# Kernel tuning notes

Measured on AMD Instinct MI355X. Metric: run time of the kernel, lower is better.

## Reference

```python
import jax, jax.numpy as jnp
import numpy as np

N_TERMS = 26000
N_EDGES = 120000
BATCH = 64
N_FEAT = 14          # n_base_models + 4
GO_EMB = 8
HID = 64
IN_DIM = N_FEAT + GO_EMB  # 22


def setup_inputs() -> dict:
    key = jax.random.key(0)
    ks = jax.random.split(key, 12)
    s = 0.05
    return {
        "x": jax.random.normal(ks[0], (BATCH, N_TERMS, N_FEAT), jnp.float32),
        "edge_index": jax.random.randint(ks[1], (2, N_EDGES), 0, N_TERMS, jnp.int32),
        "term_indices": jnp.arange(N_TERMS, dtype=jnp.int32),
        "emb_table": jax.random.normal(ks[2], (N_TERMS, GO_EMB), jnp.float32),
        "W1": jax.random.normal(ks[3], (HID, IN_DIM), jnp.float32) * s,
        "b1": jnp.zeros((HID,), jnp.float32),
        "W2": jax.random.normal(ks[4], (HID, HID), jnp.float32) * s,
        "b2": jnp.zeros((HID,), jnp.float32),
        "W3": jax.random.normal(ks[5], (HID // 2, HID), jnp.float32) * s,
        "b3": jnp.zeros((HID // 2,), jnp.float32),
        "Wout": jax.random.normal(ks[6], (1, HID // 2), jnp.float32) * s,
        "bout": jnp.zeros((1,), jnp.float32),
    }


def _go_conv(x, row, col, deg_inv, W, b):
    # x: [B, N, C]. Mean-aggregate neighbor features (col -> row), add self, linear.
    agg = jnp.zeros_like(x).at[:, row].add(x[:, col])        # scatter_add over edges
    agg = agg * deg_inv[None, :, None]
    return jnp.einsum('bnc,oc->bno', x + agg, W) + b


def reference(x, edge_index, term_indices, emb_table, W1, b1, W2, b2, W3, b3, Wout, bout):
    B, N, _ = x.shape
    row, col = edge_index[0], edge_index[1]
    deg = jnp.zeros((N,), x.dtype).at[row].add(1.0)
    deg_inv = 1.0 / jnp.clip(deg, 1.0)

    go_emb = emb_table[term_indices]                          # [N, GO_EMB]
    h = jnp.concatenate([x, jnp.broadcast_to(go_emb[None], (B, N, go_emb.shape[-1]))], axis=-1)

    h = jax.nn.relu(_go_conv(h, row, col, deg_inv, W1, b1))   # dropout: eval mode (identity)
    h = jax.nn.relu(_go_conv(h, row, col, deg_inv, W2, b2))
    h = jax.nn.relu(_go_conv(h, row, col, deg_inv, W3, b3))
    out = jax.nn.sigmoid(jnp.einsum('bnc,oc->bno', h, Wout) + bout)  # [B, N, 1]
    return out[..., 0]
```

## Files before the change

kernel.cpp:

```cpp
#include <hip/hip_runtime.h>
#include <stdint.h>

static constexpr int NT = 26000;
static constexpr int NE = 120000;

typedef __attribute__((ext_vector_type(8))) short short8;
typedef __attribute__((ext_vector_type(4))) float f32x4;
typedef __attribute__((ext_vector_type(4))) unsigned int u32x4;

__device__ __forceinline__ int rfl(int v){ return __builtin_amdgcn_readfirstlane(v); }

__device__ __forceinline__ float bf_lo(uint32_t u){ union{uint32_t u; float f;} a; a.u = u<<16; return a.f; }
__device__ __forceinline__ float bf_hi(uint32_t u){ union{uint32_t u; float f;} a; a.u = u & 0xffff0000u; return a.f; }
__device__ __forceinline__ uint32_t f2b(float f){ union{float f; uint32_t u;} a; a.f=f; return (a.u + 0x7fffu + ((a.u>>16)&1u))>>16; }

__device__ __forceinline__ void nts4(uint8_t* p, uint32_t a, uint32_t b, uint32_t c, uint32_t d){
  u32x4 v; v.x=a; v.y=b; v.z=c; v.w=d;
  __builtin_nontemporal_store(v, reinterpret_cast<u32x4*>(p));
}

__global__ __launch_bounds__(256) void k_zero_deg(int* __restrict__ deg){
  int i = blockIdx.x*256 + threadIdx.x;
  if (i < NT) deg[i] = 0;
}
__global__ __launch_bounds__(256) void k_count(const int* __restrict__ ei, int* __restrict__ deg){
  int e = blockIdx.x*256 + threadIdx.x;
  if (e < NE) atomicAdd(&deg[ei[e]], 1);
}
__global__ __launch_bounds__(1024) void k_scan(const int* __restrict__ deg, int* __restrict__ rp,
                                               int* __restrict__ cur){
  __shared__ int part[1024];
  const int t = threadIdx.x;
  const int CH = (NT + 1023)/1024;
  const int base = t*CH;
  int sum = 0;
  for (int i=0;i<CH;i++){
    int idx=base+i;
    if (idx<NT){ int d = deg[idx]; sum += (d<=4)?4:((d+3)&~3); }
  }
  part[t] = sum;
  __syncthreads();
  for (int off=1; off<1024; off<<=1){
    int v = (t>=off) ? part[t-off] : 0;
    __syncthreads();
    part[t] += v;
    __syncthreads();
  }
  int run = (t==0) ? 0 : part[t-1];
  for (int i=0;i<CH;i++){
    int idx = base+i;
    if (idx<NT){
      int d = deg[idx];
      int slot = (d<=4)?4:((d+3)&~3);
      rp[idx] = run; cur[idx] = run;
      run += slot;
    }
  }
  if (t==1023) rp[NT] = part[1023];
}
__global__ __launch_bounds__(256) void k_init(uint32_t* __restrict__ zp, uint32_t* __restrict__ cols32,
                                              float* __restrict__ scP, float* __restrict__ scQ,
                                              float* __restrict__ scY){
  int i = blockIdx.x*256 + threadIdx.x;
  if (i < 1024) zp[i] = 0;
  else if (i < 1024 + 112004) cols32[i-1024] = 0x65906590u;
  if (i < 2){ scP[NT*2+i] = 0.f; scQ[NT*2+i] = 0.f; scY[NT*2+i] = 0.f; }
}
__global__ __launch_bounds__(256) void k_fill(const int* __restrict__ ei, int* __restrict__ cur,
                                              uint16_t* __restrict__ cols){
  int e = blockIdx.x*256 + threadIdx.x;
  if (e < NE){
    int r = ei[e];
    int pos = atomicAdd(&cur[r], 1);
    cols[pos] = (uint16_t)ei[NE + e];
  }
}
__global__ __launch_bounds__(256) void k_prepw(const float* __restrict__ W1, const float* __restrict__ W2,
                                               const float* __restrict__ W3,
                                               uint16_t* __restrict__ Wt1, uint16_t* __restrict__ Wt2,
                                               uint16_t* __restrict__ Wt3){
  for (int idx = threadIdx.x; idx < 8192; idx += 256){
    if (idx < 2048){
      int o = idx >> 5, k = idx & 31;
      Wt1[idx] = (uint16_t)((k < 22) ? f2b(W1[o*22 + k]) : 0);
    } else if (idx < 6144){
      int j = idx - 2048;
      Wt2[j] = (uint16_t)f2b(W2[j]);
    } else {
      int j = idx - 6144;
      Wt3[j] = (uint16_t)f2b(W3[j]);
    }
  }
}

__global__ __launch_bounds__(256) void k_build_h0(const float* __restrict__ x, const int* __restrict__ tidx,
                                                  const float* __restrict__ emb,
                                                  uint8_t* __restrict__ p8, float* __restrict__ scP){
  __shared__ float red[2][16][16];
  __shared__ float sinv[2][16];
  const int t  = threadIdx.x;
  const int ni = t & 15;
  const int n  = blockIdx.x*16 + ni;
  const int r  = t >> 4;
  const float* er = emb + (size_t)tidx[n]*8;
  float ev[8];
  #pragma unroll
  for (int i=0;i<8;i++) ev[i]=er[i];

  float v[2][32];
  #pragma unroll
  for (int rt=0; rt<2; rt++){
    const int b = r + rt*16;
    const float* xr = x + ((size_t)b*NT + n)*14;
    float m = 0.f;
    #pragma unroll
    for (int i=0;i<14;i++){ float a=xr[i]; v[rt][i]=a; m=fmaxf(m,fabsf(a)); }
    #pragma unroll
    for (int i=0;i<8;i++){ float a=ev[i]; v[rt][14+i]=a; m=fmaxf(m,fabsf(a)); }
    #pragma unroll
    for (int i=22;i<32;i++) v[rt][i]=0.f;
    red[rt][r][ni] = m;
  }
  __syncthreads();
  if (t < 32){
    int rt = t >> 4, nn = t & 15;
    float mm = 0.f;
    #pragma unroll
    for (int i=0;i<16;i++) mm = fmaxf(mm, red[rt][i][nn]);
    sinv[rt][nn] = (mm > 0.f) ? 127.0f/mm : 0.f;
    scP[(size_t)(blockIdx.x*16+nn)*2 + rt] = mm * (1.0f/127.0f);
  }
  __syncthreads();

  uint8_t* dst = p8 + (size_t)n*1024;
  #pragma unroll
  for (int rt=0; rt<2; rt++){
    const float inv = sinv[rt][ni];
    uint32_t pk[8];
    #pragma unroll
    for (int u=0;u<8;u++){
      uint32_t w = 0;
      #pragma unroll
      for (int j=0;j<4;j++){
        int q = __float2int_rn(v[rt][u*4+j]*inv) + 128;
        q = q < 0 ? 0 : (q > 255 ? 255 : q);
        w |= (uint32_t)q << (8*j);
      }
      pk[u] = w;
    }
    nts4(dst + rt*512 + r*32,      pk[0],pk[1],pk[2],pk[3]);
    nts4(dst + rt*512 + r*32 + 16, pk[4],pk[5],pk[6],pk[7]);
  }
}

template<int KS> struct VecT;
template<> struct VecT<2>{ using T = uint4; };
template<> struct VecT<1>{ using T = uint2; };

__device__ __forceinline__ void dq_u(float* a, uint32_t u, float s){
  a[0] += s*(float)(u & 0xffu);
  a[1] += s*(float)((u>>8) & 0xffu);
  a[2] += s*(float)((u>>16) & 0xffu);
  a[3] += s*(float)(u>>24);
}
__device__ __forceinline__ void dq_s(float* a, uint32_t u, float s){
  a[0] += s*(float)(int8_t)(u & 0xff);
  a[1] += s*(float)(int8_t)((u>>8) & 0xff);
  a[2] += s*(float)(int8_t)((u>>16) & 0xff);
  a[3] += s*(float)(int8_t)(u>>24);
}
template<int KS, bool SG>
__device__ __forceinline__ void dqv(float (&acc)[KS][8], const typename VecT<KS>::T& v, float s){
  if constexpr (KS==2){
    if constexpr (SG){ dq_s(&acc[0][0],v.x,s); dq_s(&acc[0][4],v.y,s); dq_s(&acc[1][0],v.z,s); dq_s(&acc[1][4],v.w,s); }
    else             { dq_u(&acc[0][0],v.x,s); dq_u(&acc[0][4],v.y,s); dq_u(&acc[1][0],v.z,s); dq_u(&acc[1][4],v.w,s); }
  } else {
    if constexpr (SG){ dq_s(&acc[0][0],v.x,s); dq_s(&acc[0][4],v.y,s); }
    else             { dq_u(&acc[0][0],v.x,s); dq_u(&acc[0][4],v.y,s); }
  }
}

template<int KS, int STRB, int MODE>
__device__ __forceinline__ float aggregate_q(float (&acc)[KS][8], float& sumS,
    const uint8_t* __restrict__ hin, const uint8_t* __restrict__ zp8,
    const float* __restrict__ sc,
    const int* __restrict__ rp, const int* __restrict__ cur,
    const uint16_t* __restrict__ cols, int node, uint32_t offB, int rt)
{
  using V = typename VecT<KS>::T;
  constexpr bool SG = (MODE==2);
  const int e0 = rfl(rp[node]);
  const int e1 = rfl(rp[node+1]);
  const int dg = rfl(cur[node]) - e0;

  uint2 cc0 = *reinterpret_cast<const uint2*>(cols + e0);
  int a0 = rfl(cc0.x), a1 = rfl(cc0.y);
  int c0 = a0 & 0xffff, c1 = (a0>>16) & 0xffff, c2 = a1 & 0xffff, c3 = (a1>>16) & 0xffff;
  auto bp = [&](int c)->const uint8_t*{ return (c < NT) ? (hin + (size_t)c*STRB) : zp8; };

  V v0 = *reinterpret_cast<const V*>(bp(c0) + offB); float s0 = sc[c0*2+rt];
  V v1 = *reinterpret_cast<const V*>(bp(c1) + offB); float s1 = sc[c1*2+rt];
  V v2 = *reinterpret_cast<const V*>(bp(c2) + offB); float s2 = sc[c2*2+rt];
  V v3 = *reinterpret_cast<const V*>(bp(c3) + offB); float s3 = sc[c3*2+rt];
  V ow = *reinterpret_cast<const V*>(hin + (size_t)node*STRB + offB);
  float so = sc[node*2+rt];
  uint2 ccA = *reinterpret_cast<const uint2*>(cols + e0 + 4);

  const float degf = (float)(dg > 1 ? dg : 1);
  #pragma unroll
  for (int ks=0;ks<KS;ks++)
    #pragma unroll
    for (int j=0;j<8;j++) acc[ks][j]=0.f;
  dqv<KS,SG>(acc, ow, so*degf);
  if constexpr (MODE==1) sumS = so*degf;

  for (int e = e0; e < e1; e += 4){
    uint2 ccN = *reinterpret_cast<const uint2*>(cols + e + 8);
    int p0 = rfl(ccA.x), p1 = rfl(ccA.y);
    int n0 = (e+4 < e1) ? (p0 & 0xffff)         : NT;
    int n1 = (e+5 < e1) ? ((p0 >> 16) & 0xffff) : NT;
    int n2 = (e+6 < e1) ? (p1 & 0xffff)         : NT;
    int n3 = (e+7 < e1) ? ((p1 >> 16) & 0xffff) : NT;
    dqv<KS,SG>(acc, v0, s0); if constexpr (MODE==1) sumS += s0;
    v0 = *reinterpret_cast<const V*>(bp(n0) + offB); s0 = sc[n0*2+rt];
    dqv<KS,SG>(acc, v1, s1); if constexpr (MODE==1) sumS += s1;
    v1 = *reinterpret_cast<const V*>(bp(n1) + offB); s1 = sc[n1*2+rt];
    dqv<KS,SG>(acc, v2, s2); if constexpr (MODE==1) sumS += s2;
    v2 = *reinterpret_cast<const V*>(bp(n2) + offB); s2 = sc[n2*2+rt];
    dqv<KS,SG>(acc, v3, s3); if constexpr (MODE==1) sumS += s3;
    v3 = *reinterpret_cast<const V*>(bp(n3) + offB); s3 = sc[n3*2+rt];
    ccA = ccN;
  }
  return 1.0f / degf;
}

__global__ __launch_bounds__(256, 8) void k_layer1(
    const uint8_t* __restrict__ pin, const float* __restrict__ scP,
    uint8_t* __restrict__ qout, float* __restrict__ scQ,
    const int* __restrict__ rp, const int* __restrict__ cur,
    const uint16_t* __restrict__ cols, const uint8_t* __restrict__ zp8,
    const uint16_t* __restrict__ Wt, const float* __restrict__ bias)
{
  const int t=threadIdx.x, lane=t&63, w=t>>6, l15=lane&15, lg=lane>>4;
  const int rt = w & 1;
  const int node = blockIdx.x*2 + (w>>1);

  const uint32_t offB = (uint32_t)(rt*512 + l15*32 + lg*8);

  float acc[1][8]; float sumS = 0.f;
  const float di = aggregate_q<1,1024,1>(acc, sumS, pin, zp8, scP, rp, cur, cols, node, offB, rt);
  const float corr = 128.0f * sumS;

  short8 bfrag;
  #pragma unroll
  for (int j=0;j<8;j++) bfrag[j] = (short)f2b((acc[0][j] - corr)*di);

  float av[4][4];
  float m = 0.f;
  #pragma unroll
  for (int ot=0;ot<4;ot++){
    const int o0 = ot*16;
    short8 af = *reinterpret_cast<const short8*>(Wt + (o0 + l15)*32 + lg*8);
    f32x4 d = *reinterpret_cast<const f32x4*>(bias + o0 + lg*4);
    d = __builtin_amdgcn_mfma_f32_16x16x32_bf16(af, bfrag, d, 0,0,0);
    #pragma unroll
    for (int j=0;j<4;j++){
      float v = fmaxf(d[j], 0.f);
      av[ot][j] = v;
      m = fmaxf(m, v);
    }
  }
  #pragma unroll
  for (int sh=1; sh<64; sh<<=1) m = fmaxf(m, __shfl_xor(m, sh, 64));
  const float inv = (m > 0.f) ? 255.0f/m : 0.f;

  uint8_t* base = qout + (size_t)node*2048 + rt*1024 + l15*64;
  #pragma unroll
  for (int ot=0;ot<4;ot++){
    uint32_t pk = 0;
    #pragma unroll
    for (int j=0;j<4;j++){
      int q = __float2int_rn(av[ot][j]*inv);
      q = q > 255 ? 255 : q;
      pk |= (uint32_t)q << (8*j);
    }
    uint32_t boff = ((((ot&1)<<1)|(lg>>1))<<4) + ((ot>>1)<<3) + ((lg&1)<<2);
    __builtin_nontemporal_store(pk, reinterpret_cast<uint32_t*>(base + boff));
  }
  if (lane == 0) scQ[node*2+rt] = m * (1.0f/255.0f);
}

__global__ __launch_bounds__(256, 6) void k_l2g3(
    const uint8_t* __restrict__ qin, const float* __restrict__ scQ,
    uint8_t* __restrict__ yout, float* __restrict__ scY,
    const int* __restrict__ rp, const int* __restrict__ cur,
    const uint16_t* __restrict__ cols, const uint8_t* __restrict__ zp8,
    const uint16_t* __restrict__ Wt2, const float* __restrict__ bias,
    const uint16_t* __restrict__ Wt3)
{
  __shared__ uint32_t lt[4*512];
  const int t=threadIdx.x, lane=t&63, w=t>>6, l15=lane&15, lg=lane>>4;
  const int rt = w & 1;
  const int node = blockIdx.x*2 + (w>>1);

  const uint32_t offB = (uint32_t)(rt*1024 + l15*64 + lg*16);

  float acc[2][8]; float dummy;
  const float di = aggregate_q<2,2048,0>(acc, dummy, qin, zp8, scQ, rp, cur, cols, node, offB, rt);

  short8 bfrag[2];
  #pragma unroll
  for (int ks=0;ks<2;ks++){
    short8 bf;
    #pragma unroll
    for (int j=0;j<8;j++) bf[j] = (short)f2b(acc[ks][j]*di);
    bfrag[ks]=bf;
  }

  uint32_t* L = lt + w*512;
  #pragma unroll
  for (int ot=0;ot<4;ot++){
    const int o0 = ot*16;
    short8 af0 = *reinterpret_cast<const short8*>(Wt2 + (o0 + l15)*64 + lg*8);
    short8 af1 = *reinterpret_cast<const short8*>(Wt2 + (o0 + l15)*64 + 32 + lg*8);
    f32x4 d = *reinterpret_cast<const f32x4*>(bias + o0 + lg*4);
    d = __builtin_amdgcn_mfma_f32_16x16x32_bf16(af0, bfrag[0], d, 0,0,0);
    d = __builtin_amdgcn_mfma_f32_16x16x32_bf16(af1, bfrag[1], d, 0,0,0);
    float a0=fmaxf(d[0],0.f), a1=fmaxf(d[1],0.f), a2=fmaxf(d[2],0.f), a3=fmaxf(d[3],0.f);
    *reinterpret_cast<uint2*>(L + ot*128 + l15*8 + lg*2) =
        make_uint2(f2b(a0) | (f2b(a1)<<16), f2b(a2) | (f2b(a3)<<16));
  }

  short8 b3f[2];
  #pragma unroll
  for (int ks=0;ks<2;ks++)
    b3f[ks] = *reinterpret_cast<const short8*>(L + (ks*2+(lg>>1))*128 + l15*8 + (lg&1)*4);

  float dd[2][4];
  float m = 0.f;
  #pragma unroll
  for (int ot=0;ot<2;ot++){
    const int o0 = ot*16;
    short8 af0 = *reinterpret_cast<const short8*>(Wt3 + (o0 + l15)*64 + lg*8);
    short8 af1 = *reinterpret_cast<const short8*>(Wt3 + (o0 + l15)*64 + 32 + lg*8);
    f32x4 d = {0.f,0.f,0.f,0.f};
    d = __builtin_amdgcn_mfma_f32_16x16x32_bf16(af0, b3f[0], d, 0,0,0);
    d = __builtin_amdgcn_mfma_f32_16x16x32_bf16(af1, b3f[1], d, 0,0,0);
    #pragma unroll
    for (int j=0;j<4;j++){
      dd[ot][j] = d[j];
      m = fmaxf(m, fabsf(d[j]));
    }
  }
  #pragma unroll
  for (int sh=1; sh<64; sh<<=1) m = fmaxf(m, __shfl_xor(m, sh, 64));
  const float inv = (m > 0.f) ? 127.0f/m : 0.f;

  uint8_t* base = yout + (size_t)node*1024 + rt*512 + l15*32;
  #pragma unroll
  for (int ot=0;ot<2;ot++){
    uint32_t pk = 0;
    #pragma unroll
    for (int j=0;j<4;j++){
      int q = __float2int_rn(dd[ot][j]*inv);
      pk |= (uint32_t)(q & 0xff) << (8*j);
    }
    uint32_t boff = (((ot<<1)|(lg>>1))<<3) + ((lg&1)<<2);
    __builtin_nontemporal_store(pk, reinterpret_cast<uint32_t*>(base + boff));
  }
  if (lane == 0) scY[node*2+rt] = m * (1.0f/127.0f);
}

__global__ __launch_bounds__(256, 8) void k_fin(
    const uint8_t* __restrict__ yin, const float* __restrict__ scY,
    const int* __restrict__ rp, const int* __restrict__ cur,
    const uint16_t* __restrict__ cols, const uint8_t* __restrict__ zp8,
    const float* __restrict__ b3, const float* __restrict__ Wo, const float* __restrict__ bo,
    float* __restrict__ tmp)
{
  const int t=threadIdx.x, lane=t&63, w=t>>6, l15=lane&15, lg=lane>>4;
  const int rt = w & 1;
  const int node = blockIdx.x*2 + (w>>1);

  const uint32_t offB = (uint32_t)(rt*512 + l15*32 + lg*8);

  float acc[1][8]; float dummy;
  const float di = aggregate_q<1,1024,2>(acc, dummy, yin, zp8, scY, rp, cur, cols, node, offB, rt);

  const int k0 = lg*8;
  f32x4 bA = *reinterpret_cast<const f32x4*>(b3 + k0);
  f32x4 bB = *reinterpret_cast<const f32x4*>(b3 + k0 + 4);
  f32x4 wA = *reinterpret_cast<const f32x4*>(Wo + k0);
  f32x4 wB = *reinterpret_cast<const f32x4*>(Wo + k0 + 4);
  float z = 0.f;
  #pragma unroll
  for (int j=0;j<4;j++){
    z += fmaxf(acc[0][j]  *di + bA[j], 0.f) * wA[j];
    z += fmaxf(acc[0][4+j]*di + bB[j], 0.f) * wB[j];
  }
  z += __shfl_xor(z, 16, 64);
  z += __shfl_xor(z, 32, 64);
  if (lg == 0){
    float sg = 1.f/(1.f + expf(-(z + bo[0])));
    tmp[(size_t)node*32 + rt*16 + l15] = sg;
  }
}

__global__ __launch_bounds__(256) void k_tr(const float* __restrict__ tmp, float* __restrict__ out){
  int n = blockIdx.x*256 + threadIdx.x;
  if (n < NT){
    f32x4 r[8];
    #pragma unroll
    for (int q=0;q<8;q++) r[q] = *reinterpret_cast<const f32x4*>(tmp + (size_t)n*32 + q*4);
    #pragma unroll
    for (int q=0;q<8;q++)
      #pragma unroll
      for (int j=0;j<4;j++)
        out[(size_t)(q*4+j)*NT + n] = r[q][j];
  }
}

static constexpr size_t OFF_P    = 0;
static constexpr size_t OFF_Q    = 26624000;
static constexpr size_t OFF_TMP  = 79872000;
static constexpr size_t OFF_ZP   = 83200000;
static constexpr size_t OFF_WT1  = OFF_ZP  + 4096;
static constexpr size_t OFF_WT2  = OFF_WT1 + 4096;
static constexpr size_t OFF_WT3  = OFF_WT2 + 8192;
static constexpr size_t OFF_SCP  = OFF_WT3 + 4096;
static constexpr size_t OFF_SCQ  = OFF_SCP + 208016;
static constexpr size_t OFF_SCY  = OFF_SCQ + 208016;
static constexpr size_t OFF_DEG  = OFF_SCY + 208016;
static constexpr size_t OFF_RP   = OFF_DEG + 104000;
static constexpr size_t OFF_CUR  = OFF_RP  + 104016;
static constexpr size_t OFF_COLS = OFF_CUR + 104000;
static constexpr size_t WS_NEED  = OFF_COLS + 448016;

extern "C" void kernel_launch(void* const* d_in, const int* in_sizes, int n_in,
                              void* d_out, int out_size, void* d_ws, size_t ws_size,
                              hipStream_t stream)
{
  const float* x    = (const float*)d_in[0];
  const int*   ei   = (const int*)  d_in[1];
  const int*   tidx = (const int*)  d_in[2];
  const float* emb  = (const float*)d_in[3];
  const float* W1   = (const float*)d_in[4];
  const float* b1   = (const float*)d_in[5];
  const float* W2   = (const float*)d_in[6];
  const float* b2   = (const float*)d_in[7];
  const float* W3   = (const float*)d_in[8];
  const float* b3   = (const float*)d_in[9];
  const float* Wo   = (const float*)d_in[10];
  const float* bo   = (const float*)d_in[11];
  float* out = (float*)d_out;

  if (ws_size < WS_NEED) return;

  char* ws = (char*)d_ws;
  uint8_t*  P    = (uint8_t*) (ws + OFF_P);
  uint8_t*  Y3   = (uint8_t*) (ws + OFF_P);
  uint8_t*  Q    = (uint8_t*) (ws + OFF_Q);
  float*    tmpf = (float*)   (ws + OFF_TMP);
  uint32_t* zp   = (uint32_t*)(ws + OFF_ZP);
  uint8_t*  zp8  = (uint8_t*) (ws + OFF_ZP);
  uint16_t* Wt1  = (uint16_t*)(ws + OFF_WT1);
  uint16_t* Wt2  = (uint16_t*)(ws + OFF_WT2);
  uint16_t* Wt3  = (uint16_t*)(ws + OFF_WT3);
  float*    scP  = (float*)   (ws + OFF_SCP);
  float*    scQ  = (float*)   (ws + OFF_SCQ);
  float*    scY  = (float*)   (ws + OFF_SCY);
  int*      deg  = (int*)     (ws + OFF_DEG);
  int*      rp   = (int*)     (ws + OFF_RP);
  int*      cur  = (int*)     (ws + OFF_CUR);
  uint16_t* cols = (uint16_t*)(ws + OFF_COLS);

  k_zero_deg<<<(NT+255)/256, 256, 0, stream>>>(deg);
  k_count   <<<(NE+255)/256, 256, 0, stream>>>(ei, deg);
  k_scan    <<<1, 1024, 0, stream>>>(deg, rp, cur);
  k_init    <<<442, 256, 0, stream>>>(zp, (uint32_t*)cols, scP, scQ, scY);
  k_fill    <<<(NE+255)/256, 256, 0, stream>>>(ei, cur, cols);
  k_prepw   <<<1, 256, 0, stream>>>(W1, W2, W3, Wt1, Wt2, Wt3);

  for (int ch = 0; ch < 2; ch++){
    k_build_h0<<<NT/16, 256, 0, stream>>>(x + (size_t)ch*32*NT*14, tidx, emb, P, scP);
    k_layer1<<<NT/2, 256, 0, stream>>>(P, scP, Q, scQ, rp, cur, cols, zp8, Wt1, b1);
    k_l2g3  <<<NT/2, 256, 0, stream>>>(Q, scQ, Y3, scY, rp, cur, cols, zp8, Wt2, b2, Wt3);
    k_fin   <<<NT/2, 256, 0, stream>>>(Y3, scY, rp, cur, cols, zp8, b3, Wo, bo, tmpf);
    k_tr    <<<(NT+255)/256, 256, 0, stream>>>(tmpf, out + (size_t)ch*32*NT);
  }
}
```

Before: 501.0 us.

## Merge batch chunks into single launches and store first 16 neighbors per node in fixed slots

New measurement: 507.8 us. Within noise of the previous version (+1.4%).

```diff
diff --git a/kernel.cpp b/kernel.cpp
--- a/kernel.cpp
+++ b/kernel.cpp
@@ -8,10 +8,10 @@
 typedef __attribute__((ext_vector_type(4))) float f32x4;
 typedef __attribute__((ext_vector_type(4))) unsigned int u32x4;
 
+static constexpr int SCS = 52004;
+
 __device__ __forceinline__ int rfl(int v){ return __builtin_amdgcn_readfirstlane(v); }
 
-__device__ __forceinline__ float bf_lo(uint32_t u){ union{uint32_t u; float f;} a; a.u = u<<16; return a.f; }
-__device__ __forceinline__ float bf_hi(uint32_t u){ union{uint32_t u; float f;} a; a.u = u & 0xffff0000u; return a.f; }
 __device__ __forceinline__ uint32_t f2b(float f){ union{float f; uint32_t u;} a; a.f=f; return (a.u + 0x7fffu + ((a.u>>16)&1u))>>16; }
 
 __device__ __forceinline__ void nts4(uint8_t* p, uint32_t a, uint32_t b, uint32_t c, uint32_t d){
@@ -59,20 +59,31 @@
   if (t==1023) rp[NT] = part[1023];
 }
 __global__ __launch_bounds__(256) void k_init(uint32_t* __restrict__ zp, uint32_t* __restrict__ cols32,
+                                              uint32_t* __restrict__ cols2_32,
                                               float* __restrict__ scP, float* __restrict__ scQ,
                                               float* __restrict__ scY){
   int i = blockIdx.x*256 + threadIdx.x;
   if (i < 1024) zp[i] = 0;
-  else if (i < 1024 + 112004) cols32[i-1024] = 0x65906590u;
-  if (i < 2){ scP[NT*2+i] = 0.f; scQ[NT*2+i] = 0.f; scY[NT*2+i] = 0.f; }
+  else if (i < 113028) cols32[i-1024] = 0x65906590u;
+  else if (i < 321028) cols2_32[i-113028] = 0x65906590u;
+  if (i < 4){
+    int ch = i>>1, j = i&1;
+    scP[ch*SCS + NT*2 + j] = 0.f;
+    scQ[ch*SCS + NT*2 + j] = 0.f;
+    scY[ch*SCS + NT*2 + j] = 0.f;
+  }
 }
 __global__ __launch_bounds__(256) void k_fill(const int* __restrict__ ei, int* __restrict__ cur,
-                                              uint16_t* __restrict__ cols){
+                                              const int* __restrict__ rp,
+                                              uint16_t* __restrict__ cols, uint16_t* __restrict__ cols2){
   int e = blockIdx.x*256 + threadIdx.x;
   if (e < NE){
     int r = ei[e];
     int pos = atomicAdd(&cur[r], 1);
-    cols[pos] = (uint16_t)ei[NE + e];
+    int slot = pos - rp[r];
+    uint16_t c = (uint16_t)ei[NE + e];
+    if (slot < 16) cols2[r*16 + slot] = c;
+    else           cols[pos] = c;
   }
 }
 __global__ __launch_bounds__(256) void k_prepw(const float* __restrict__ W1, const float* __restrict__ W2,
@@ -98,9 +109,16 @@
                                                   uint8_t* __restrict__ p8, float* __restrict__ scP){
   __shared__ float red[2][16][16];
   __shared__ float sinv[2][16];
+  const int nb16 = NT/16;
+  const int ch = (blockIdx.x >= nb16) ? 1 : 0;
+  const int bi = blockIdx.x - ch*nb16;
+  const float* xc = x + (size_t)ch*32*NT*14;
+  uint8_t* p8c = p8 + (size_t)ch*NT*1024;
+  float* scc = scP + (size_t)ch*SCS;
+
   const int t  = threadIdx.x;
   const int ni = t & 15;
-  const int n  = blockIdx.x*16 + ni;
+  const int n  = bi*16 + ni;
   const int r  = t >> 4;
   const float* er = emb + (size_t)tidx[n]*8;
   float ev[8];
@@ -111,7 +129,7 @@
   #pragma unroll
   for (int rt=0; rt<2; rt++){
     const int b = r + rt*16;
-    const float* xr = x + ((size_t)b*NT + n)*14;
+    const float* xr = xc + ((size_t)b*NT + n)*14;
     float m = 0.f;
     #pragma unroll
     for (int i=0;i<14;i++){ float a=xr[i]; v[rt][i]=a; m=fmaxf(m,fabsf(a)); }
@@ -128,11 +146,11 @@
     #pragma unroll
     for (int i=0;i<16;i++) mm = fmaxf(mm, red[rt][i][nn]);
     sinv[rt][nn] = (mm > 0.f) ? 127.0f/mm : 0.f;
-    scP[(size_t)(blockIdx.x*16+nn)*2 + rt] = mm * (1.0f/127.0f);
+    scc[(size_t)(bi*16+nn)*2 + rt] = mm * (1.0f/127.0f);
   }
   __syncthreads();
 
-  uint8_t* dst = p8 + (size_t)n*1024;
+  uint8_t* dst = p8c + (size_t)n*1024;
   #pragma unroll
   for (int rt=0; rt<2; rt++){
     const float inv = sinv[rt][ni];
@@ -181,32 +199,37 @@
 }
 
 template<int KS, int STRB, int MODE>
-__device__ __forceinline__ float aggregate_q(float (&acc)[KS][8], float& sumS,
+__device__ __forceinline__ float aggregate8(float (&acc)[KS][8], float& sumS,
     const uint8_t* __restrict__ hin, const uint8_t* __restrict__ zp8,
     const float* __restrict__ sc,
-    const int* __restrict__ rp, const int* __restrict__ cur,
-    const uint16_t* __restrict__ cols, int node, uint32_t offB, int rt)
+    const int* __restrict__ deg, const int* __restrict__ rp,
+    const uint16_t* __restrict__ cols, const uint16_t* __restrict__ cols2,
+    int node, uint32_t offB, int rt)
 {
   using V = typename VecT<KS>::T;
   constexpr bool SG = (MODE==2);
-  const int e0 = rfl(rp[node]);
-  const int e1 = rfl(rp[node+1]);
-  const int dg = rfl(cur[node]) - e0;
-
-  uint2 cc0 = *reinterpret_cast<const uint2*>(cols + e0);
-  int a0 = rfl(cc0.x), a1 = rfl(cc0.y);
-  int c0 = a0 & 0xffff, c1 = (a0>>16) & 0xffff, c2 = a1 & 0xffff, c3 = (a1>>16) & 0xffff;
   auto bp = [&](int c)->const uint8_t*{ return (c < NT) ? (hin + (size_t)c*STRB) : zp8; };
 
-  V v0 = *reinterpret_cast<const V*>(bp(c0) + offB); float s0 = sc[c0*2+rt];
-  V v1 = *reinterpret_cast<const V*>(bp(c1) + offB); float s1 = sc[c1*2+rt];
-  V v2 = *reinterpret_cast<const V*>(bp(c2) + offB); float s2 = sc[c2*2+rt];
-  V v3 = *reinterpret_cast<const V*>(bp(c3) + offB); float s3 = sc[c3*2+rt];
+  const uint4 cc0 = *reinterpret_cast<const uint4*>(cols2 + node*16);
+  const uint4 cc1 = *reinterpret_cast<const uint4*>(cols2 + node*16 + 8);
+  const int dg = rfl(deg[node]);
   V ow = *reinterpret_cast<const V*>(hin + (size_t)node*STRB + offB);
-  float so = sc[node*2+rt];
-  uint2 ccA = *reinterpret_cast<const uint2*>(cols + e0 + 4);
-
-  const float degf = (float)(dg > 1 ? dg : 1);
+  const float so = sc[node*2+rt];
+
+  int c0 = rfl(cc0.x)&0xffff, c1 = (rfl(cc0.x)>>16)&0xffff;
+  int c2 = rfl(cc0.y)&0xffff, c3 = (rfl(cc0.y)>>16)&0xffff;
+  int c4 = rfl(cc0.z)&0xffff, c5 = (rfl(cc0.z)>>16)&0xffff;
+  int c6 = rfl(cc0.w)&0xffff, c7 = (rfl(cc0.w)>>16)&0xffff;
+  V v0 = *reinterpret_cast<const V*>(bp(c0)+offB); float s0 = sc[c0*2+rt];
+  V v1 = *reinterpret_cast<const V*>(bp(c1)+offB); float s1 = sc[c1*2+rt];
+  V v2 = *reinterpret_cast<const V*>(bp(c2)+offB); float s2 = sc[c2*2+rt];
+  V v3 = *reinterpret_cast<const V*>(bp(c3)+offB); float s3 = sc[c3*2+rt];
+  V v4 = *reinterpret_cast<const V*>(bp(c4)+offB); float s4 = sc[c4*2+rt];
+  V v5 = *reinterpret_cast<const V*>(bp(c5)+offB); float s5 = sc[c5*2+rt];
+  V v6 = *reinterpret_cast<const V*>(bp(c6)+offB); float s6 = sc[c6*2+rt];
+  V v7 = *reinterpret_cast<const V*>(bp(c7)+offB); float s7 = sc[c7*2+rt];
+
+  const float degf = (dg > 1) ? (float)dg : 1.0f;
   #pragma unroll
   for (int ks=0;ks<KS;ks++)
     #pragma unroll
@@ -214,41 +237,77 @@
   dqv<KS,SG>(acc, ow, so*degf);
   if constexpr (MODE==1) sumS = so*degf;
 
-  for (int e = e0; e < e1; e += 4){
-    uint2 ccN = *reinterpret_cast<const uint2*>(cols + e + 8);
-    int p0 = rfl(ccA.x), p1 = rfl(ccA.y);
-    int n0 = (e+4 < e1) ? (p0 & 0xffff)         : NT;
-    int n1 = (e+5 < e1) ? ((p0 >> 16) & 0xffff) : NT;
-    int n2 = (e+6 < e1) ? (p1 & 0xffff)         : NT;
-    int n3 = (e+7 < e1) ? ((p1 >> 16) & 0xffff) : NT;
-    dqv<KS,SG>(acc, v0, s0); if constexpr (MODE==1) sumS += s0;
-    v0 = *reinterpret_cast<const V*>(bp(n0) + offB); s0 = sc[n0*2+rt];
-    dqv<KS,SG>(acc, v1, s1); if constexpr (MODE==1) sumS += s1;
-    v1 = *reinterpret_cast<const V*>(bp(n1) + offB); s1 = sc[n1*2+rt];
-    dqv<KS,SG>(acc, v2, s2); if constexpr (MODE==1) sumS += s2;
-    v2 = *reinterpret_cast<const V*>(bp(n2) + offB); s2 = sc[n2*2+rt];
-    dqv<KS,SG>(acc, v3, s3); if constexpr (MODE==1) sumS += s3;
-    v3 = *reinterpret_cast<const V*>(bp(n3) + offB); s3 = sc[n3*2+rt];
-    ccA = ccN;
+  dqv<KS,SG>(acc, v0, s0); dqv<KS,SG>(acc, v1, s1);
+  dqv<KS,SG>(acc, v2, s2); dqv<KS,SG>(acc, v3, s3);
+  if constexpr (MODE==1) sumS += s0+s1+s2+s3;
+  if (dg > 4){
+    dqv<KS,SG>(acc, v4, s4); dqv<KS,SG>(acc, v5, s5);
+    dqv<KS,SG>(acc, v6, s6); dqv<KS,SG>(acc, v7, s7);
+    if constexpr (MODE==1) sumS += s4+s5+s6+s7;
+  }
+  if (dg > 8){
+    int c8  = rfl(cc1.x)&0xffff, c9  = (rfl(cc1.x)>>16)&0xffff;
+    int c10 = rfl(cc1.y)&0xffff, c11 = (rfl(cc1.y)>>16)&0xffff;
+    V w0 = *reinterpret_cast<const V*>(bp(c8)+offB);  float t0 = sc[c8*2+rt];
+    V w1 = *reinterpret_cast<const V*>(bp(c9)+offB);  float t1 = sc[c9*2+rt];
+    V w2 = *reinterpret_cast<const V*>(bp(c10)+offB); float t2 = sc[c10*2+rt];
+    V w3 = *reinterpret_cast<const V*>(bp(c11)+offB); float t3 = sc[c11*2+rt];
+    dqv<KS,SG>(acc, w0, t0); dqv<KS,SG>(acc, w1, t1);
+    dqv<KS,SG>(acc, w2, t2); dqv<KS,SG>(acc, w3, t3);
+    if constexpr (MODE==1) sumS += t0+t1+t2+t3;
+    if (dg > 12){
+      int c12 = rfl(cc1.z)&0xffff, c13 = (rfl(cc1.z)>>16)&0xffff;
+      int c14 = rfl(cc1.w)&0xffff, c15 = (rfl(cc1.w)>>16)&0xffff;
+      V y0 = *reinterpret_cast<const V*>(bp(c12)+offB); float u0 = sc[c12*2+rt];
+      V y1 = *reinterpret_cast<const V*>(bp(c13)+offB); float u1 = sc[c13*2+rt];
+      V y2 = *reinterpret_cast<const V*>(bp(c14)+offB); float u2 = sc[c14*2+rt];
+      V y3 = *reinterpret_cast<const V*>(bp(c15)+offB); float u3 = sc[c15*2+rt];
+      dqv<KS,SG>(acc, y0, u0); dqv<KS,SG>(acc, y1, u1);
+      dqv<KS,SG>(acc, y2, u2); dqv<KS,SG>(acc, y3, u3);
+      if constexpr (MODE==1) sumS += u0+u1+u2+u3;
+      if (dg > 16){
+        const int e0 = rfl(rp[node]);
+        const int slots = (dg+3)&~3;
+        for (int e = 16; e < slots; e += 4){
+          uint2 cx = *reinterpret_cast<const uint2*>(cols + e0 + e);
+          int d0 = rfl(cx.x)&0xffff, d1 = (rfl(cx.x)>>16)&0xffff;
+          int d2 = rfl(cx.y)&0xffff, d3 = (rfl(cx.y)>>16)&0xffff;
+          V z0 = *reinterpret_cast<const V*>(bp(d0)+offB); float q0 = sc[d0*2+rt];
+          V z1 = *reinterpret_cast<const V*>(bp(d1)+offB); float q1 = sc[d1*2+rt];
+          V z2 = *reinterpret_cast<const V*>(bp(d2)+offB); float q2 = sc[d2*2+rt];
+          V z3 = *reinterpret_cast<const V*>(bp(d3)+offB); float q3 = sc[d3*2+rt];
+          dqv<KS,SG>(acc, z0, q0); dqv<KS,SG>(acc, z1, q1);
+          dqv<KS,SG>(acc, z2, q2); dqv<KS,SG>(acc, z3, q3);
+          if constexpr (MODE==1) sumS += q0+q1+q2+q3;
+        }
+      }
+    }
   }
   return 1.0f / degf;
 }
 
-__global__ __launch_bounds__(256, 8) void k_layer1(
+__global__ __launch_bounds__(256, 6) void k_layer1(
     const uint8_t* __restrict__ pin, const float* __restrict__ scP,
     uint8_t* __restrict__ qout, float* __restrict__ scQ,
-    const int* __restrict__ rp, const int* __restrict__ cur,
-    const uint16_t* __restrict__ cols, const uint8_t* __restrict__ zp8,
+    const int* __restrict__ deg, const int* __restrict__ rp,
+    const uint16_t* __restrict__ cols, const uint16_t* __restrict__ cols2,
+    const uint8_t* __restrict__ zp8,
     const uint16_t* __restrict__ Wt, const float* __restrict__ bias)
 {
   const int t=threadIdx.x, lane=t&63, w=t>>6, l15=lane&15, lg=lane>>4;
   const int rt = w & 1;
-  const int node = blockIdx.x*2 + (w>>1);
+  const int idx = blockIdx.x*2 + (w>>1);
+  const int ch = (idx >= NT) ? 1 : 0;
+  const int node = idx - ch*NT;
+  const uint8_t* pc = pin + (size_t)ch*NT*1024;
+  uint8_t* qc = qout + (size_t)ch*NT*2048;
+  const float* scp = scP + (size_t)ch*SCS;
+  float* scq = scQ + (size_t)ch*SCS;
 
   const uint32_t offB = (uint32_t)(rt*512 + l15*32 + lg*8);
 
   float acc[1][8]; float sumS = 0.f;
-  const float di = aggregate_q<1,1024,1>(acc, sumS, pin, zp8, scP, rp, cur, cols, node, offB, rt);
+  const float di = aggregate8<1,1024,1>(acc, sumS, pc, zp8, scp, deg, rp, cols, cols2, node, offB, rt);
   const float corr = 128.0f * sumS;
 
   short8 bfrag;
@@ -274,7 +333,7 @@
   for (int sh=1; sh<64; sh<<=1) m = fmaxf(m, __shfl_xor(m, sh, 64));
   const float inv = (m > 0.f) ? 255.0f/m : 0.f;
 
-  uint8_t* base = qout + (size_t)node*2048 + rt*1024 + l15*64;
+  uint8_t* base = qc + (size_t)node*2048 + rt*1024 + l15*64;
   #pragma unroll
   for (int ot=0;ot<4;ot++){
     uint32_t pk = 0;
@@ -287,26 +346,33 @@
     uint32_t boff = ((((ot&1)<<1)|(lg>>1))<<4) + ((ot>>1)<<3) + ((lg&1)<<2);
     __builtin_nontemporal_store(pk, reinterpret_cast<uint32_t*>(base + boff));
   }
-  if (lane == 0) scQ[node*2+rt] = m * (1.0f/255.0f);
-}
-
-__global__ __launch_bounds__(256, 6) void k_l2g3(
+  if (lane == 0) scq[node*2+rt] = m * (1.0f/255.0f);
+}
+
+__global__ __launch_bounds__(256, 4) void k_l2g3(
     const uint8_t* __restrict__ qin, const float* __restrict__ scQ,
     uint8_t* __restrict__ yout, float* __restrict__ scY,
-    const int* __restrict__ rp, const int* __restrict__ cur,
-    const uint16_t* __restrict__ cols, const uint8_t* __restrict__ zp8,
+    const int* __restrict__ deg, const int* __restrict__ rp,
+    const uint16_t* __restrict__ cols, const uint16_t* __restrict__ cols2,
+    const uint8_t* __restrict__ zp8,
     const uint16_t* __restrict__ Wt2, const float* __restrict__ bias,
     const uint16_t* __restrict__ Wt3)
 {
   __shared__ uint32_t lt[4*512];
   const int t=threadIdx.x, lane=t&63, w=t>>6, l15=lane&15, lg=lane>>4;
   const int rt = w & 1;
-  const int node = blockIdx.x*2 + (w>>1);
+  const int idx = blockIdx.x*2 + (w>>1);
+  const int ch = (idx >= NT) ? 1 : 0;
+  const int node = idx - ch*NT;
+  const uint8_t* qc = qin + (size_t)ch*NT*2048;
+  uint8_t* yc = yout + (size_t)ch*NT*1024;
+  const float* scq = scQ + (size_t)ch*SCS;
+  float* scy = scY + (size_t)ch*SCS;
 
   const uint32_t offB = (uint32_t)(rt*1024 + l15*64 + lg*16);
 
   float acc[2][8]; float dummy;
-  const float di = aggregate_q<2,2048,0>(acc, dummy, qin, zp8, scQ, rp, cur, cols, node, offB, rt);
+  const float di = aggregate8<2,2048,0>(acc, dummy, qc, zp8, scq, deg, rp, cols, cols2, node, offB, rt);
 
   short8 bfrag[2];
   #pragma unroll
@@ -356,7 +422,7 @@
   for (int sh=1; sh<64; sh<<=1) m = fmaxf(m, __shfl_xor(m, sh, 64));
   const float inv = (m > 0.f) ? 127.0f/m : 0.f;
 
-  uint8_t* base = yout + (size_t)node*1024 + rt*512 + l15*32;
+  uint8_t* base = yc + (size_t)node*1024 + rt*512 + l15*32;
   #pragma unroll
   for (int ot=0;ot<2;ot++){
     uint32_t pk = 0;
@@ -368,24 +434,29 @@
     uint32_t boff = (((ot<<1)|(lg>>1))<<3) + ((lg&1)<<2);
     __builtin_nontemporal_store(pk, reinterpret_cast<uint32_t*>(base + boff));
   }
-  if (lane == 0) scY[node*2+rt] = m * (1.0f/127.0f);
-}
-
-__global__ __launch_bounds__(256, 8) void k_fin(
+  if (lane == 0) scy[node*2+rt] = m * (1.0f/127.0f);
+}
+
+__global__ __launch_bounds__(256, 6) void k_fin(
     const uint8_t* __restrict__ yin, const float* __restrict__ scY,
-    const int* __restrict__ rp, const int* __restrict__ cur,
-    const uint16_t* __restrict__ cols, const uint8_t* __restrict__ zp8,
+    const int* __restrict__ deg, const int* __restrict__ rp,
+    const uint16_t* __restrict__ cols, const uint16_t* __restrict__ cols2,
+    const uint8_t* __restrict__ zp8,
     const float* __restrict__ b3, const float* __restrict__ Wo, const float* __restrict__ bo,
     float* __restrict__ tmp)
 {
   const int t=threadIdx.x, lane=t&63, w=t>>6, l15=lane&15, lg=lane>>4;
   const int rt = w & 1;
-  const int node = blockIdx.x*2 + (w>>1);
+  const int idx = blockIdx.x*2 + (w>>1);
+  const int ch = (idx >= NT) ? 1 : 0;
+  const int node = idx - ch*NT;
+  const uint8_t* yc = yin + (size_t)ch*NT*1024;
+  const float* scy = scY + (size_t)ch*SCS;
 
   const uint32_t offB = (uint32_t)(rt*512 + l15*32 + lg*8);
 
   float acc[1][8]; float dummy;
-  const float di = aggregate_q<1,1024,2>(acc, dummy, yin, zp8, scY, rp, cur, cols, node, offB, rt);
+  const float di = aggregate8<1,1024,2>(acc, dummy, yc, zp8, scy, deg, rp, cols, cols2, node, offB, rt);
 
   const int k0 = lg*8;
   f32x4 bA = *reinterpret_cast<const f32x4*>(b3 + k0);
@@ -402,39 +473,45 @@
   z += __shfl_xor(z, 32, 64);
   if (lg == 0){
     float sg = 1.f/(1.f + expf(-(z + bo[0])));
-    tmp[(size_t)node*32 + rt*16 + l15] = sg;
+    tmp[(size_t)ch*NT*32 + (size_t)node*32 + rt*16 + l15] = sg;
   }
 }
 
 __global__ __launch_bounds__(256) void k_tr(const float* __restrict__ tmp, float* __restrict__ out){
-  int n = blockIdx.x*256 + threadIdx.x;
+  const int nb = (NT + 255)/256;
+  const int ch = (blockIdx.x >= nb) ? 1 : 0;
+  const int bi = blockIdx.x - ch*nb;
+  int n = bi*256 + threadIdx.x;
   if (n < NT){
+    const float* tc = tmp + (size_t)ch*NT*32;
+    float* oc = out + (size_t)ch*32*NT;
     f32x4 r[8];
     #pragma unroll
-    for (int q=0;q<8;q++) r[q] = *reinterpret_cast<const f32x4*>(tmp + (size_t)n*32 + q*4);
+    for (int q=0;q<8;q++) r[q] = *reinterpret_cast<const f32x4*>(tc + (size_t)n*32 + q*4);
     #pragma unroll
     for (int q=0;q<8;q++)
       #pragma unroll
       for (int j=0;j<4;j++)
-        out[(size_t)(q*4+j)*NT + n] = r[q][j];
-  }
-}
-
-static constexpr size_t OFF_P    = 0;
-static constexpr size_t OFF_Q    = 26624000;
-static constexpr size_t OFF_TMP  = 79872000;
-static constexpr size_t OFF_ZP   = 83200000;
-static constexpr size_t OFF_WT1  = OFF_ZP  + 4096;
-static constexpr size_t OFF_WT2  = OFF_WT1 + 4096;
-static constexpr size_t OFF_WT3  = OFF_WT2 + 8192;
-static constexpr size_t OFF_SCP  = OFF_WT3 + 4096;
-static constexpr size_t OFF_SCQ  = OFF_SCP + 208016;
-static constexpr size_t OFF_SCY  = OFF_SCQ + 208016;
-static constexpr size_t OFF_DEG  = OFF_SCY + 208016;
-static constexpr size_t OFF_RP   = OFF_DEG + 104000;
-static constexpr size_t OFF_CUR  = OFF_RP  + 104016;
-static constexpr size_t OFF_COLS = OFF_CUR + 104000;
-static constexpr size_t WS_NEED  = OFF_COLS + 448016;
+        oc[(size_t)(q*4+j)*NT + n] = r[q][j];
+  }
+}
+
+static constexpr size_t OFF_P     = 0;
+static constexpr size_t OFF_Q     = 53248000;
+static constexpr size_t OFF_TMP   = 159744000;
+static constexpr size_t OFF_ZP    = 166400000;
+static constexpr size_t OFF_WT1   = 166404096;
+static constexpr size_t OFF_WT2   = 166408192;
+static constexpr size_t OFF_WT3   = 166416384;
+static constexpr size_t OFF_SCP   = 166420480;
+static constexpr size_t OFF_SCQ   = 166836512;
+static constexpr size_t OFF_SCY   = 167252544;
+static constexpr size_t OFF_DEG   = 167668576;
+static constexpr size_t OFF_RP    = 167772576;
+static constexpr size_t OFF_CUR   = 167876592;
+static constexpr size_t OFF_COLS  = 167980592;
+static constexpr size_t OFF_COLS2 = 168428608;
+static constexpr size_t WS_NEED   = 169260608;
 
 extern "C" void kernel_launch(void* const* d_in, const int* in_sizes, int n_in,
                               void* d_out, int out_size, void* d_ws, size_t ws_size,
@@ -457,35 +534,34 @@
   if (ws_size < WS_NEED) return;
 
   char* ws = (char*)d_ws;
-  uint8_t*  P    = (uint8_t*) (ws + OFF_P);
-  uint8_t*  Y3   = (uint8_t*) (ws + OFF_P);
-  uint8_t*  Q    = (uint8_t*) (ws + OFF_Q);
-  float*    tmpf = (float*)   (ws + OFF_TMP);
-  uint32_t* zp   = (uint32_t*)(ws + OFF_ZP);
-  uint8_t*  zp8  = (uint8_t*) (ws + OFF_ZP);
-  uint16_t* Wt1  = (uint16_t*)(ws + OFF_WT1);
-  uint16_t* Wt2  = (uint16_t*)(ws + OFF_WT2);
-  uint16_t* Wt3  = (uint16_t*)(ws + OFF_WT3);
-  float*    scP  = (float*)   (ws + OFF_SCP);
-  float*    scQ  = (float*)   (ws + OFF_SCQ);
-  float*    scY  = (float*)   (ws + OFF_SCY);
-  int*      deg  = (int*)     (ws + OFF_DEG);
-  int*      rp   = (int*)     (ws + OFF_RP);
-  int*      cur  = (int*)     (ws + OFF_CUR);
-  uint16_t* cols = (uint16_t*)(ws + OFF_COLS);
+  uint8_t*  P     = (uint8_t*) (ws + OFF_P);
+  uint8_t*  Y3    = (uint8_t*) (ws + OFF_P);
+  uint8_t*  Q     = (uint8_t*) (ws + OFF_Q);
+  float*    tmpf  = (float*)   (ws + OFF_TMP);
+  uint32_t* zp    = (uint32_t*)(ws + OFF_ZP);
+  uint8_t*  zp8   = (uint8_t*) (ws + OFF_ZP);
+  uint16_t* Wt1   = (uint16_t*)(ws + OFF_WT1);
+  uint16_t* Wt2   = (uint16_t*)(ws + OFF_WT2);
+  uint16_t* Wt3   = (uint16_t*)(ws + OFF_WT3);
+  float*    scP   = (float*)   (ws + OFF_SCP);
+  float*    scQ   = (float*)   (ws + OFF_SCQ);
+  float*    scY   = (float*)   (ws + OFF_SCY);
+  int*      deg   = (int*)     (ws + OFF_DEG);
+  int*      rp    = (int*)     (ws + OFF_RP);
+  int*      cur   = (int*)     (ws + OFF_CUR);
+  uint16_t* cols  = (uint16_t*)(ws + OFF_COLS);
+  uint16_t* cols2 = (uint16_t*)(ws + OFF_COLS2);
 
   k_zero_deg<<<(NT+255)/256, 256, 0, stream>>>(deg);
   k_count   <<<(NE+255)/256, 256, 0, stream>>>(ei, deg);
   k_scan    <<<1, 1024, 0, stream>>>(deg, rp, cur);
-  k_init    <<<442, 256, 0, stream>>>(zp, (uint32_t*)cols, scP, scQ, scY);
-  k_fill    <<<(NE+255)/256, 256, 0, stream>>>(ei, cur, cols);
+  k_init    <<<1255, 256, 0, stream>>>(zp, (uint32_t*)cols, (uint32_t*)cols2, scP, scQ, scY);
+  k_fill    <<<(NE+255)/256, 256, 0, stream>>>(ei, cur, rp, cols, cols2);
   k_prepw   <<<1, 256, 0, stream>>>(W1, W2, W3, Wt1, Wt2, Wt3);
 
-  for (int ch = 0; ch < 2; ch++){
-    k_build_h0<<<NT/16, 256, 0, stream>>>(x + (size_t)ch*32*NT*14, tidx, emb, P, scP);
-    k_layer1<<<NT/2, 256, 0, stream>>>(P, scP, Q, scQ, rp, cur, cols, zp8, Wt1, b1);
-    k_l2g3  <<<NT/2, 256, 0, stream>>>(Q, scQ, Y3, scY, rp, cur, cols, zp8, Wt2, b2, Wt3);
-    k_fin   <<<NT/2, 256, 0, stream>>>(Y3, scY, rp, cur, cols, zp8, b3, Wo, bo, tmpf);
-    k_tr    <<<(NT+255)/256, 256, 0, stream>>>(tmpf, out + (size_t)ch*32*NT);
-  }
-}
+  k_build_h0<<<2*(NT/16), 256, 0, stream>>>(x, tidx, emb, P, scP);
+  k_layer1  <<<NT, 256, 0, stream>>>(P, scP, Q, scQ, deg, rp, cols, cols2, zp8, Wt1, b1);
+  k_l2g3    <<<NT, 256, 0, stream>>>(Q, scQ, Y3, scY, deg, rp, cols, cols2, zp8, Wt2, b2, Wt3);
+  k_fin     <<<NT, 256, 0, stream>>>(Y3, scY, deg, rp, cols, cols2, zp8, b3, Wo, bo, tmpf);
+  k_tr      <<<2*((NT+255)/256), 256, 0, stream>>>(tmpf, out);
+}
```
